# Kernel tuning notes

Hardware: AMD Instinct MI355X
Metric: run time of the kernel (lower is better)

Reference implementation:

```python
import jax, jax.numpy as jnp
import numpy as np
import math

SEGMENT_LENGTHS = [2048, 4096, 8192]
DILATION_RATES = [1, 2, 4]


def setup_inputs() -> dict:
    key = jax.random.key(0)
    kq, kk, kv = jax.random.split(key, 3)
    b, n, h, d = 2, 8192, 32, 128
    q = jax.random.normal(kq, (b, n, h, d), dtype=jnp.float32)
    k = jax.random.normal(kk, (b, n, h, d), dtype=jnp.float32)
    v = jax.random.normal(kv, (b, n, h, d), dtype=jnp.float32)
    return {"q": q, "k": k, "v": v}


def _dilated_attention(q, k, v):
    # Faithful translation of _compute_dilated_attention.
    # NOTE: torch.matmul on (b, S, h, d) with transpose(-2, -1) contracts over
    # head_dim d and yields (b, S, h, h) scores: heads attend to heads at a
    # single (possibly dilated) key position. We reproduce that exactly.
    b, n, h, d = q.shape
    scale = 1.0 / math.sqrt(d)
    out = jnp.zeros_like(q)
    for seg_len, dil in zip(SEGMENT_LENGTHS, DILATION_RATES):
        if seg_len > n:
            continue
        n_seg = n // seg_len
        cov = n_seg * seg_len
        # (b, n_seg, seg_len, h, d)
        qs = q[:, :cov].reshape(b, n_seg, seg_len, h, d)
        if dil == 1:
            ks = k[:, :cov].reshape(b, n_seg, seg_len, h, d)
            vs = v[:, :cov].reshape(b, n_seg, seg_len, h, d)
        else:
            # idx[g, i] = g*seg_len + i*dil, clamped to n-1 (matches the loop)
            idx = (jnp.arange(n_seg)[:, None] * seg_len
                   + jnp.arange(seg_len)[None, :] * dil)
            idx = jnp.minimum(idx, n - 1)  # (n_seg, seg_len)
            ks = k[:, idx]  # (b, n_seg, seg_len, h, d)
            vs = v[:, idx]
        scores = jnp.einsum('bgsid,bgsjd->bgsij', qs, ks) * scale  # (b,g,s,h,h)
        attn = jax.nn.softmax(scores, axis=-1)
        res = jnp.einsum('bgsij,bgsjd->bgsid', attn, vs)
        # later configs overwrite earlier ones, as in the torch loop
        out = out.at[:, :cov].set(res.reshape(b, cov, h, d))
    return out


def reference(q, k, v):
    # world_size == 1 -> hierarchy level 1 -> _local_forward with all heads
    # local, which is just _compute_dilated_attention.
    return _dilated_attention(q, k, v)
```

## Files before the change

### kernel.cpp

```cpp
#include <hip/hip_runtime.h>
#include <hip/hip_bf16.h>

typedef __attribute__((ext_vector_type(4))) float f32x4;
typedef __attribute__((ext_vector_type(8))) __bf16 bf16x8;

#define NCTX 8192
#define DH 128
#define ROWE 4096
#define SC2 0.12751705766482797f
#define KSTR 136
#define PSTR 40
#define OSTR 132
#define BUFS (32*KSTR)

__device__ __forceinline__ unsigned f2bf(float x) {
  union { float f; unsigned u; } un; un.f = x;
  return (un.u + 0x7FFFu + ((un.u >> 16) & 1u)) >> 16;
}
__device__ __forceinline__ unsigned pk2(float a, float b) {
  float2 t; t.x = a; t.y = b;
  union { __hip_bfloat162 h; unsigned u; } un;
  un.h = __float22bfloat162_rn(t);
  return un.u;
}

template<bool NT>
__device__ __forceinline__ void stage_row(const float* __restrict__ src,
                                          unsigned short* dst, int lane) {
  const int jb = lane >> 5, d = 4 * (lane & 31);
#pragma unroll
  for (int half = 0; half < 2; ++half) {
    f32x4 x[8];
#pragma unroll
    for (int ch = 0; ch < 8; ++ch) {
      const f32x4* p = reinterpret_cast<const f32x4*>(src + 4*lane + 256*(half*8 + ch));
      x[ch] = NT ? __builtin_nontemporal_load(p) : *p;
    }
#pragma unroll
    for (int ch = 0; ch < 8; ++ch) {
      const int j = jb + 2*(half*8 + ch);
      uint2 wv;
      wv.x = pk2(x[ch][0], x[ch][1]);
      wv.y = pk2(x[ch][2], x[ch][3]);
      *reinterpret_cast<uint2*>(&dst[j*KSTR + d]) = wv;
    }
  }
}

__global__ __launch_bounds__(256, 3) void hda(
    const float* __restrict__ q, const float* __restrict__ kg,
    const float* __restrict__ v, float* __restrict__ out)
{
  extern __shared__ __align__(16) unsigned short lds[];

  const int tid  = threadIdx.x;
  const int w    = tid >> 6;
  const int lane = tid & 63;
  const int c = lane & 15;
  const int g = lane >> 4;
  const int jb = lane >> 5, dcol = 4 * (lane & 31);

  const int pos = blockIdx.x * 4 + w;
  const int b = pos >> 13;
  const int s = pos & (NCTX - 1);
  const int s0 = (blockIdx.x * 4) & (NCTX - 1);
  const bool shared_kv = (s0 >= 2048);

  const float* qb_ = q  + (size_t)b * NCTX * ROWE;
  const float* kb_ = kg + (size_t)b * NCTX * ROWE;
  const float* vb_ = v  + (size_t)b * NCTX * ROWE;
  float*       op  = out + ((size_t)b * NCTX + s) * ROWE;

  unsigned short* sb = lds + w * BUFS;
  const unsigned short* kbuf = shared_kv ? (lds + 4*BUFS) : sb;
  const unsigned short* vbuf = shared_kv ? (lds + 5*BUFS) : sb;

  if (shared_kv) {
    const float* kr8 = kb_ + (size_t)(NCTX - 1) * ROWE;
    const float* vr8 = vb_ + (size_t)(NCTX - 1) * ROWE;
    const int d = 4 * (tid & 31), jj = tid >> 5;
#pragma unroll
    for (int ch = 0; ch < 4; ++ch) {
      const int fo = 4*tid + 1024*ch;
      const int j  = jj + 8*ch;
      f32x4 xk = *reinterpret_cast<const f32x4*>(kr8 + fo);
      f32x4 xv = *reinterpret_cast<const f32x4*>(vr8 + fo);
      uint2 wk, wv2;
      wk.x  = pk2(xk[0], xk[1]); wk.y  = pk2(xk[2], xk[3]);
      wv2.x = pk2(xv[0], xv[1]); wv2.y = pk2(xv[2], xv[3]);
      *reinterpret_cast<uint2*>(&lds[4*BUFS + j*KSTR + d]) = wk;
      *reinterpret_cast<uint2*>(&lds[5*BUFS + j*KSTR + d]) = wv2;
    }
    __syncthreads();
  }

  stage_row<true>(qb_ + (size_t)s * ROWE, sb, lane);
  bf16x8 qa[2][4];
#pragma unroll
  for (int t = 0; t < 2; ++t)
#pragma unroll
    for (int ks = 0; ks < 4; ++ks)
      qa[t][ks] = *reinterpret_cast<const bf16x8*>(&sb[(t*16 + c)*KSTR + ks*32 + g*8]);

  const float* vsrc = vb_ + (size_t)(4*s) * ROWE;
  if (!shared_kv)
    stage_row<false>(kb_ + (size_t)(4*s) * ROWE, sb, lane);
  bf16x8 kf[2][4];
#pragma unroll
  for (int t = 0; t < 2; ++t)
#pragma unroll
    for (int ks = 0; ks < 4; ++ks)
      kf[t][ks] = *reinterpret_cast<const bf16x8*>(&kbuf[(t*16 + c)*KSTR + ks*32 + g*8]);

  f32x4 vx[8];
  if (!shared_kv) {
#pragma unroll
    for (int ch = 0; ch < 8; ++ch)
      vx[ch] = *reinterpret_cast<const f32x4*>(vsrc + 4*lane + 256*ch);
    __builtin_amdgcn_sched_barrier(0);
  }

  f32x4 S[2][2];
#pragma unroll
  for (int it = 0; it < 2; ++it)
#pragma unroll
    for (int jt = 0; jt < 2; ++jt) {
      f32x4 acc = (f32x4)0.0f;
#pragma unroll
      for (int ks = 0; ks < 4; ++ks)
        acc = __builtin_amdgcn_mfma_f32_16x16x32_bf16(qa[it][ks], kf[jt][ks], acc, 0, 0, 0);
      S[it][jt] = acc;
    }

  if (!shared_kv) {
#pragma unroll
    for (int ch = 0; ch < 8; ++ch) {
      uint2 wv;
      wv.x = pk2(vx[ch][0], vx[ch][1]);
      wv.y = pk2(vx[ch][2], vx[ch][3]);
      *reinterpret_cast<uint2*>(&sb[(jb + 2*ch)*KSTR + dcol]) = wv;
    }
#pragma unroll
    for (int ch = 0; ch < 8; ++ch)
      vx[ch] = *reinterpret_cast<const f32x4*>(vsrc + 4*lane + 256*(8 + ch));
    __builtin_amdgcn_sched_barrier(0);
  }

  float p[2][2][4], inv[2][4];
#pragma unroll
  for (int it = 0; it < 2; ++it) {
    float ls[4] = {0.f, 0.f, 0.f, 0.f};
#pragma unroll
    for (int jt = 0; jt < 2; ++jt)
#pragma unroll
      for (int rr = 0; rr < 4; ++rr) {
        float e = exp2f(S[it][jt][rr] * SC2);
        p[it][jt][rr] = e;
        ls[rr] += e;
      }
#pragma unroll
    for (int m = 1; m <= 8; m <<= 1)
#pragma unroll
      for (int rr = 0; rr < 4; ++rr)
        ls[rr] += __shfl_xor(ls[rr], m);
#pragma unroll
    for (int rr = 0; rr < 4; ++rr) inv[it][rr] = 1.0f / ls[rr];
  }

  if (!shared_kv) {
#pragma unroll
    for (int ch = 0; ch < 8; ++ch) {
      uint2 wv;
      wv.x = pk2(vx[ch][0], vx[ch][1]);
      wv.y = pk2(vx[ch][2], vx[ch][3]);
      *reinterpret_cast<uint2*>(&sb[(jb + 2*(8 + ch))*KSTR + dcol]) = wv;
    }
  }

  bf16x8 va[8];
#pragma unroll
  for (int dt = 0; dt < 8; ++dt) {
    unsigned t0 = vbuf[(g*8 + 0)*KSTR + dt*16 + c];
    unsigned t1 = vbuf[(g*8 + 1)*KSTR + dt*16 + c];
    unsigned t2 = vbuf[(g*8 + 2)*KSTR + dt*16 + c];
    unsigned t3 = vbuf[(g*8 + 3)*KSTR + dt*16 + c];
    unsigned t4 = vbuf[(g*8 + 4)*KSTR + dt*16 + c];
    unsigned t5 = vbuf[(g*8 + 5)*KSTR + dt*16 + c];
    unsigned t6 = vbuf[(g*8 + 6)*KSTR + dt*16 + c];
    unsigned t7 = vbuf[(g*8 + 7)*KSTR + dt*16 + c];
    union { unsigned u[4]; bf16x8 f; } un;
    un.u[0] = t0 | (t1 << 16); un.u[1] = t2 | (t3 << 16);
    un.u[2] = t4 | (t5 << 16); un.u[3] = t6 | (t7 << 16);
    va[dt] = un.f;
  }

#pragma unroll
  for (int it = 0; it < 2; ++it)
#pragma unroll
    for (int jt = 0; jt < 2; ++jt)
#pragma unroll
      for (int rr = 0; rr < 4; ++rr)
        sb[(it*16 + g*4 + rr)*PSTR + jt*16 + c] =
            (unsigned short)f2bf(p[it][jt][rr] * inv[it][rr]);

  bf16x8 pa[2];
  pa[0] = *reinterpret_cast<const bf16x8*>(&sb[c*PSTR + g*8]);
  pa[1] = *reinterpret_cast<const bf16x8*>(&sb[(16 + c)*PSTR + g*8]);

  float* ob = reinterpret_cast<float*>(sb);
#pragma unroll
  for (int it = 0; it < 2; ++it) {
    f32x4 o[8];
#pragma unroll
    for (int dt = 0; dt < 8; ++dt)
      o[dt] = __builtin_amdgcn_mfma_f32_16x16x32_bf16(va[dt], pa[it], (f32x4)0.0f, 0, 0, 0);
#pragma unroll
    for (int dt = 0; dt < 8; ++dt)
      *reinterpret_cast<f32x4*>(&ob[c*OSTR + dt*16 + g*4]) = o[dt];
#pragma unroll
    for (int ch = 0; ch < 8; ++ch) {
      const int flat = 4*lane + 256*ch;
      const int row = flat >> 7, col = flat & 127;
      f32x4 y = *reinterpret_cast<const f32x4*>(&ob[row*OSTR + col]);
      __builtin_nontemporal_store(y, reinterpret_cast<f32x4*>(op + it*2048 + flat));
    }
  }
}

extern "C" void kernel_launch(void* const* d_in, const int* in_sizes, int n_in,
                              void* d_out, int out_size, void* d_ws, size_t ws_size,
                              hipStream_t stream) {
  const float* q = (const float*)d_in[0];
  const float* k = (const float*)d_in[1];
  const float* v = (const float*)d_in[2];
  float* o = (float*)d_out;
  hda<<<dim3(4096, 1, 1), dim3(256, 1, 1), 6 * BUFS * 2, stream>>>(q, k, v, o);
}
```

Baseline: 113.5 us.

## Loop four positions per wave with double-buffered async LDS prefetch of Q

Each wave now handles four consecutive sequence positions in a loop instead of one. The Q row for the next position is prefetched straight into LDS with global_load_lds into a double buffer, overlapping its load with the current position's compute. The grid shrinks to a quarter, and LDS grows to roughly 160KB with launch bounds lowered to one block per CU. The aim is to hide Q load latency and amortise the shared K/V setup, at the cost of far less occupancy and manual vmcnt waits that must match the number of outstanding loads.

New measurement: 129.5 us. +14.1%, slower.

```diff
diff --git a/kernel.cpp b/kernel.cpp
--- a/kernel.cpp
+++ b/kernel.cpp
@@ -11,7 +11,11 @@
 #define KSTR 136
 #define PSTR 40
 #define OSTR 132
-#define BUFS (32*KSTR)
+#define QSTRIDE 17408
+#define KVOFF (8*QSTRIDE)
+#define LDS_TOTAL (KVOFF + 2*8704)
+#define VOFF_B 8704
+#define OOFF_B 2560
 
 __device__ __forceinline__ unsigned f2bf(float x) {
   union { float f; unsigned u; } un; un.f = x;
@@ -23,8 +27,13 @@
   un.h = __float22bfloat162_rn(t);
   return un.u;
 }
-
-template<bool NT>
+__device__ __forceinline__ bf16x8 mk8(f32x4 x, f32x4 y) {
+  union { unsigned u[4]; bf16x8 f; } un;
+  un.u[0] = pk2(x[0], x[1]); un.u[1] = pk2(x[2], x[3]);
+  un.u[2] = pk2(y[0], y[1]); un.u[3] = pk2(y[2], y[3]);
+  return un.f;
+}
+
 __device__ __forceinline__ void stage_row(const float* __restrict__ src,
                                           unsigned short* dst, int lane) {
   const int jb = lane >> 5, d = 4 * (lane & 31);
@@ -32,10 +41,8 @@
   for (int half = 0; half < 2; ++half) {
     f32x4 x[8];
 #pragma unroll
-    for (int ch = 0; ch < 8; ++ch) {
-      const f32x4* p = reinterpret_cast<const f32x4*>(src + 4*lane + 256*(half*8 + ch));
-      x[ch] = NT ? __builtin_nontemporal_load(p) : *p;
-    }
+    for (int ch = 0; ch < 8; ++ch)
+      x[ch] = *reinterpret_cast<const f32x4*>(src + 4*lane + 256*(half*8 + ch));
 #pragma unroll
     for (int ch = 0; ch < 8; ++ch) {
       const int j = jb + 2*(half*8 + ch);
@@ -47,11 +54,25 @@
   }
 }
 
-__global__ __launch_bounds__(256, 3) void hda(
+__device__ __forceinline__ void dma_q(const float* __restrict__ qsrc,
+                                      char* dst, int lane) {
+#pragma unroll
+  for (int k = 0; k < 17; ++k) {
+    const int t = (k << 6) + lane;
+    int row = (t * 993) >> 15;
+    int cg  = t - row * 33;
+    row = min(row, 31); cg = min(cg, 31);
+    __builtin_amdgcn_global_load_lds(
+        reinterpret_cast<const unsigned int*>(qsrc + row*128 + cg*4),
+        reinterpret_cast<unsigned int*>(dst + (k << 10)), 16, 0, 0);
+  }
+}
+
+__global__ __launch_bounds__(256, 1) void hda(
     const float* __restrict__ q, const float* __restrict__ kg,
     const float* __restrict__ v, float* __restrict__ out)
 {
-  extern __shared__ __align__(16) unsigned short lds[];
+  extern __shared__ __align__(16) char lds[];
 
   const int tid  = threadIdx.x;
   const int w    = tid >> 6;
@@ -60,25 +81,25 @@
   const int g = lane >> 4;
   const int jb = lane >> 5, dcol = 4 * (lane & 31);
 
-  const int pos = blockIdx.x * 4 + w;
-  const int b = pos >> 13;
-  const int s = pos & (NCTX - 1);
-  const int s0 = (blockIdx.x * 4) & (NCTX - 1);
+  const int p0 = (blockIdx.x * 4 + w) * 4;
+  const int b  = p0 >> 13;
+  const int s0 = p0 & (NCTX - 1);
   const bool shared_kv = (s0 >= 2048);
 
   const float* qb_ = q  + (size_t)b * NCTX * ROWE;
   const float* kb_ = kg + (size_t)b * NCTX * ROWE;
   const float* vb_ = v  + (size_t)b * NCTX * ROWE;
-  float*       op  = out + ((size_t)b * NCTX + s) * ROWE;
-
-  unsigned short* sb = lds + w * BUFS;
-  const unsigned short* kbuf = shared_kv ? (lds + 4*BUFS) : sb;
-  const unsigned short* vbuf = shared_kv ? (lds + 5*BUFS) : sb;
+  float*       ob_ = out + (size_t)b * NCTX * ROWE;
+
+  char* qb0 = lds + w * 2 * QSTRIDE;
+  char* qb1 = qb0 + QSTRIDE;
+  unsigned short* kvK = reinterpret_cast<unsigned short*>(lds + KVOFF);
+  unsigned short* kvV = kvK + 32 * KSTR;
 
   if (shared_kv) {
     const float* kr8 = kb_ + (size_t)(NCTX - 1) * ROWE;
     const float* vr8 = vb_ + (size_t)(NCTX - 1) * ROWE;
-    const int d = 4 * (tid & 31), jj = tid >> 5;
+    const int d0 = 4 * (tid & 31), jj = tid >> 5;
 #pragma unroll
     for (int ch = 0; ch < 4; ++ch) {
       const int fo = 4*tid + 1024*ch;
@@ -88,141 +109,166 @@
       uint2 wk, wv2;
       wk.x  = pk2(xk[0], xk[1]); wk.y  = pk2(xk[2], xk[3]);
       wv2.x = pk2(xv[0], xv[1]); wv2.y = pk2(xv[2], xv[3]);
-      *reinterpret_cast<uint2*>(&lds[4*BUFS + j*KSTR + d]) = wk;
-      *reinterpret_cast<uint2*>(&lds[5*BUFS + j*KSTR + d]) = wv2;
+      *reinterpret_cast<uint2*>(&kvK[j*KSTR + d0]) = wk;
+      *reinterpret_cast<uint2*>(&kvV[j*KSTR + d0]) = wv2;
     }
     __syncthreads();
   }
 
-  stage_row<true>(qb_ + (size_t)s * ROWE, sb, lane);
-  bf16x8 qa[2][4];
-#pragma unroll
-  for (int t = 0; t < 2; ++t)
-#pragma unroll
-    for (int ks = 0; ks < 4; ++ks)
-      qa[t][ks] = *reinterpret_cast<const bf16x8*>(&sb[(t*16 + c)*KSTR + ks*32 + g*8]);
-
-  const float* vsrc = vb_ + (size_t)(4*s) * ROWE;
-  if (!shared_kv)
-    stage_row<false>(kb_ + (size_t)(4*s) * ROWE, sb, lane);
-  bf16x8 kf[2][4];
-#pragma unroll
-  for (int t = 0; t < 2; ++t)
-#pragma unroll
-    for (int ks = 0; ks < 4; ++ks)
-      kf[t][ks] = *reinterpret_cast<const bf16x8*>(&kbuf[(t*16 + c)*KSTR + ks*32 + g*8]);
-
-  f32x4 vx[8];
-  if (!shared_kv) {
-#pragma unroll
-    for (int ch = 0; ch < 8; ++ch)
-      vx[ch] = *reinterpret_cast<const f32x4*>(vsrc + 4*lane + 256*ch);
+  dma_q(qb_ + (size_t)s0 * ROWE, qb0, lane);
+
+#pragma unroll 1
+  for (int i = 0; i < 4; ++i) {
+    const int s = s0 + i;
+    char* qcur = (i & 1) ? qb1 : qb0;
+    char* qnxt = (i & 1) ? qb0 : qb1;
+
+    if (i == 0) asm volatile("s_waitcnt vmcnt(0)" ::: "memory");
+    else        asm volatile("s_waitcnt vmcnt(16)" ::: "memory");
     __builtin_amdgcn_sched_barrier(0);
-  }
-
-  f32x4 S[2][2];
-#pragma unroll
-  for (int it = 0; it < 2; ++it)
-#pragma unroll
-    for (int jt = 0; jt < 2; ++jt) {
-      f32x4 acc = (f32x4)0.0f;
+
+    bf16x8 qa[2][4];
+#pragma unroll
+    for (int t = 0; t < 2; ++t)
+#pragma unroll
+      for (int ks = 0; ks < 4; ++ks) {
+        const int gr = (t*16 + c)*33 + ks*8 + 2*g;
+        f32x4 x = *reinterpret_cast<const f32x4*>(qcur + gr*16);
+        f32x4 y = *reinterpret_cast<const f32x4*>(qcur + gr*16 + 16);
+        qa[t][ks] = mk8(x, y);
+      }
+
+    if (i < 3)
+      dma_q(qb_ + (size_t)(s + 1) * ROWE, qnxt, lane);
+
+    unsigned short* sbK = reinterpret_cast<unsigned short*>(qcur);
+    const unsigned short* kb = shared_kv ? kvK : sbK;
+    if (!shared_kv)
+      stage_row(kb_ + (size_t)(4*s) * ROWE, sbK, lane);
+    bf16x8 kf[2][4];
+#pragma unroll
+    for (int t = 0; t < 2; ++t)
 #pragma unroll
       for (int ks = 0; ks < 4; ++ks)
-        acc = __builtin_amdgcn_mfma_f32_16x16x32_bf16(qa[it][ks], kf[jt][ks], acc, 0, 0, 0);
-      S[it][jt] = acc;
-    }
-
-  if (!shared_kv) {
-#pragma unroll
-    for (int ch = 0; ch < 8; ++ch) {
-      uint2 wv;
-      wv.x = pk2(vx[ch][0], vx[ch][1]);
-      wv.y = pk2(vx[ch][2], vx[ch][3]);
-      *reinterpret_cast<uint2*>(&sb[(jb + 2*ch)*KSTR + dcol]) = wv;
-    }
-#pragma unroll
-    for (int ch = 0; ch < 8; ++ch)
-      vx[ch] = *reinterpret_cast<const f32x4*>(vsrc + 4*lane + 256*(8 + ch));
-    __builtin_amdgcn_sched_barrier(0);
-  }
-
-  float p[2][2][4], inv[2][4];
-#pragma unroll
-  for (int it = 0; it < 2; ++it) {
-    float ls[4] = {0.f, 0.f, 0.f, 0.f};
-#pragma unroll
-    for (int jt = 0; jt < 2; ++jt)
-#pragma unroll
-      for (int rr = 0; rr < 4; ++rr) {
-        float e = exp2f(S[it][jt][rr] * SC2);
-        p[it][jt][rr] = e;
-        ls[rr] += e;
-      }
-#pragma unroll
-    for (int m = 1; m <= 8; m <<= 1)
-#pragma unroll
-      for (int rr = 0; rr < 4; ++rr)
-        ls[rr] += __shfl_xor(ls[rr], m);
-#pragma unroll
-    for (int rr = 0; rr < 4; ++rr) inv[it][rr] = 1.0f / ls[rr];
-  }
-
-  if (!shared_kv) {
-#pragma unroll
-    for (int ch = 0; ch < 8; ++ch) {
-      uint2 wv;
-      wv.x = pk2(vx[ch][0], vx[ch][1]);
-      wv.y = pk2(vx[ch][2], vx[ch][3]);
-      *reinterpret_cast<uint2*>(&sb[(jb + 2*(8 + ch))*KSTR + dcol]) = wv;
-    }
-  }
-
-  bf16x8 va[8];
-#pragma unroll
-  for (int dt = 0; dt < 8; ++dt) {
-    unsigned t0 = vbuf[(g*8 + 0)*KSTR + dt*16 + c];
-    unsigned t1 = vbuf[(g*8 + 1)*KSTR + dt*16 + c];
-    unsigned t2 = vbuf[(g*8 + 2)*KSTR + dt*16 + c];
-    unsigned t3 = vbuf[(g*8 + 3)*KSTR + dt*16 + c];
-    unsigned t4 = vbuf[(g*8 + 4)*KSTR + dt*16 + c];
-    unsigned t5 = vbuf[(g*8 + 5)*KSTR + dt*16 + c];
-    unsigned t6 = vbuf[(g*8 + 6)*KSTR + dt*16 + c];
-    unsigned t7 = vbuf[(g*8 + 7)*KSTR + dt*16 + c];
-    union { unsigned u[4]; bf16x8 f; } un;
-    un.u[0] = t0 | (t1 << 16); un.u[1] = t2 | (t3 << 16);
-    un.u[2] = t4 | (t5 << 16); un.u[3] = t6 | (t7 << 16);
-    va[dt] = un.f;
-  }
-
-#pragma unroll
-  for (int it = 0; it < 2; ++it)
-#pragma unroll
-    for (int jt = 0; jt < 2; ++jt)
-#pragma unroll
-      for (int rr = 0; rr < 4; ++rr)
-        sb[(it*16 + g*4 + rr)*PSTR + jt*16 + c] =
-            (unsigned short)f2bf(p[it][jt][rr] * inv[it][rr]);
-
-  bf16x8 pa[2];
-  pa[0] = *reinterpret_cast<const bf16x8*>(&sb[c*PSTR + g*8]);
-  pa[1] = *reinterpret_cast<const bf16x8*>(&sb[(16 + c)*PSTR + g*8]);
-
-  float* ob = reinterpret_cast<float*>(sb);
-#pragma unroll
-  for (int it = 0; it < 2; ++it) {
-    f32x4 o[8];
-#pragma unroll
-    for (int dt = 0; dt < 8; ++dt)
-      o[dt] = __builtin_amdgcn_mfma_f32_16x16x32_bf16(va[dt], pa[it], (f32x4)0.0f, 0, 0, 0);
-#pragma unroll
-    for (int dt = 0; dt < 8; ++dt)
-      *reinterpret_cast<f32x4*>(&ob[c*OSTR + dt*16 + g*4]) = o[dt];
-#pragma unroll
-    for (int ch = 0; ch < 8; ++ch) {
-      const int flat = 4*lane + 256*ch;
-      const int row = flat >> 7, col = flat & 127;
-      f32x4 y = *reinterpret_cast<const f32x4*>(&ob[row*OSTR + col]);
-      __builtin_nontemporal_store(y, reinterpret_cast<f32x4*>(op + it*2048 + flat));
+        kf[t][ks] = *reinterpret_cast<const bf16x8*>(&kb[(t*16 + c)*KSTR + ks*32 + g*8]);
+
+    const float* vsrc = vb_ + (size_t)(4*s) * ROWE;
+    unsigned short* sbV = reinterpret_cast<unsigned short*>(qcur + VOFF_B);
+    const unsigned short* vbuf = shared_kv ? kvV : sbV;
+    f32x4 vx[8];
+    if (!shared_kv) {
+#pragma unroll
+      for (int ch = 0; ch < 8; ++ch)
+        vx[ch] = *reinterpret_cast<const f32x4*>(vsrc + 4*lane + 256*ch);
+      __builtin_amdgcn_sched_barrier(0);
+    }
+
+    f32x4 S[2][2];
+#pragma unroll
+    for (int it = 0; it < 2; ++it)
+#pragma unroll
+      for (int jt = 0; jt < 2; ++jt) {
+        f32x4 acc = (f32x4)0.0f;
+#pragma unroll
+        for (int ks = 0; ks < 4; ++ks)
+          acc = __builtin_amdgcn_mfma_f32_16x16x32_bf16(qa[it][ks], kf[jt][ks], acc, 0, 0, 0);
+        S[it][jt] = acc;
+      }
+
+    if (!shared_kv) {
+#pragma unroll
+      for (int ch = 0; ch < 8; ++ch) {
+        uint2 wv;
+        wv.x = pk2(vx[ch][0], vx[ch][1]);
+        wv.y = pk2(vx[ch][2], vx[ch][3]);
+        *reinterpret_cast<uint2*>(&sbV[(jb + 2*ch)*KSTR + dcol]) = wv;
+      }
+#pragma unroll
+      for (int ch = 0; ch < 8; ++ch)
+        vx[ch] = *reinterpret_cast<const f32x4*>(vsrc + 4*lane + 256*(8 + ch));
+      __builtin_amdgcn_sched_barrier(0);
+    }
+
+    float pp[2][2][4], inv[2][4];
+#pragma unroll
+    for (int it = 0; it < 2; ++it) {
+      float ls[4] = {0.f, 0.f, 0.f, 0.f};
+#pragma unroll
+      for (int jt = 0; jt < 2; ++jt)
+#pragma unroll
+        for (int rr = 0; rr < 4; ++rr) {
+          float e = exp2f(S[it][jt][rr] * SC2);
+          pp[it][jt][rr] = e;
+          ls[rr] += e;
+        }
+#pragma unroll
+      for (int m = 1; m <= 8; m <<= 1)
+#pragma unroll
+        for (int rr = 0; rr < 4; ++rr)
+          ls[rr] += __shfl_xor(ls[rr], m);
+#pragma unroll
+      for (int rr = 0; rr < 4; ++rr) inv[it][rr] = 1.0f / ls[rr];
+    }
+
+    if (!shared_kv) {
+#pragma unroll
+      for (int ch = 0; ch < 8; ++ch) {
+        uint2 wv;
+        wv.x = pk2(vx[ch][0], vx[ch][1]);
+        wv.y = pk2(vx[ch][2], vx[ch][3]);
+        *reinterpret_cast<uint2*>(&sbV[(jb + 2*(8 + ch))*KSTR + dcol]) = wv;
+      }
+    }
+
+    bf16x8 va[8];
+#pragma unroll
+    for (int dt = 0; dt < 8; ++dt) {
+      unsigned t0 = vbuf[(g*8 + 0)*KSTR + dt*16 + c];
+      unsigned t1 = vbuf[(g*8 + 1)*KSTR + dt*16 + c];
+      unsigned t2 = vbuf[(g*8 + 2)*KSTR + dt*16 + c];
+      unsigned t3 = vbuf[(g*8 + 3)*KSTR + dt*16 + c];
+      unsigned t4 = vbuf[(g*8 + 4)*KSTR + dt*16 + c];
+      unsigned t5 = vbuf[(g*8 + 5)*KSTR + dt*16 + c];
+      unsigned t6 = vbuf[(g*8 + 6)*KSTR + dt*16 + c];
+      unsigned t7 = vbuf[(g*8 + 7)*KSTR + dt*16 + c];
+      union { unsigned u[4]; bf16x8 f; } un;
+      un.u[0] = t0 | (t1 << 16); un.u[1] = t2 | (t3 << 16);
+      un.u[2] = t4 | (t5 << 16); un.u[3] = t6 | (t7 << 16);
+      va[dt] = un.f;
+    }
+
+    unsigned short* sbP = reinterpret_cast<unsigned short*>(qcur);
+#pragma unroll
+    for (int it = 0; it < 2; ++it)
+#pragma unroll
+      for (int jt = 0; jt < 2; ++jt)
+#pragma unroll
+        for (int rr = 0; rr < 4; ++rr)
+          sbP[(it*16 + g*4 + rr)*PSTR + jt*16 + c] =
+              (unsigned short)f2bf(pp[it][jt][rr] * inv[it][rr]);
+
+    bf16x8 pa[2];
+    pa[0] = *reinterpret_cast<const bf16x8*>(&sbP[c*PSTR + g*8]);
+    pa[1] = *reinterpret_cast<const bf16x8*>(&sbP[(16 + c)*PSTR + g*8]);
+
+    float* op = ob_ + (size_t)s * ROWE;
+    float* ob = reinterpret_cast<float*>(qcur + OOFF_B);
+#pragma unroll
+    for (int it = 0; it < 2; ++it) {
+      f32x4 o[8];
+#pragma unroll
+      for (int dt = 0; dt < 8; ++dt)
+        o[dt] = __builtin_amdgcn_mfma_f32_16x16x32_bf16(va[dt], pa[it], (f32x4)0.0f, 0, 0, 0);
+#pragma unroll
+      for (int dt = 0; dt < 8; ++dt)
+        *reinterpret_cast<f32x4*>(&ob[c*OSTR + dt*16 + g*4]) = o[dt];
+#pragma unroll
+      for (int ch = 0; ch < 8; ++ch) {
+        const int flat = 4*lane + 256*ch;
+        const int row = flat >> 7, col = flat & 127;
+        f32x4 y = *reinterpret_cast<const f32x4*>(&ob[row*OSTR + col]);
+        __builtin_nontemporal_store(y, reinterpret_cast<f32x4*>(op + it*2048 + flat));
+      }
     }
   }
 }
@@ -234,5 +280,7 @@
   const float* k = (const float*)d_in[1];
   const float* v = (const float*)d_in[2];
   float* o = (float*)d_out;
-  hda<<<dim3(4096, 1, 1), dim3(256, 1, 1), 6 * BUFS * 2, stream>>>(q, k, v, o);
-}
+  hipFuncSetAttribute(reinterpret_cast<const void*>(hda),
+                      hipFuncAttributeMaxDynamicSharedMemorySize, LDS_TOTAL);
+  hda<<<dim3(1024, 1, 1), dim3(256, 1, 1), LDS_TOTAL, stream>>>(q, k, v, o);
+}
```
